# Optimization experiments

Hardware: AMD Instinct MI355X
Metric: run time of the kernel (lower is better)

The kernel has to match this reference:

```python
import jax, jax.numpy as jnp
import numpy as np

N_ACTIVE = 200000   # active voxels
GRID = 96           # spatial grid extent per axis
C = 128             # inplanes == outplanes
EPS = 1e-4          # scn BatchNormalization default eps


def _build_rulebook(n, g, seed=0):
    """Submanifold 3x3x3 rulebook: for each of 27 offsets, pairs (in_site, out_site)
    where coord[in] = coord[out] + offset and both sites are active. Padded to
    length n with dummy index n."""
    rng = np.random.default_rng(seed)
    lin = rng.choice(g ** 3, size=n, replace=False)
    coords = np.stack(np.unravel_index(lin, (g, g, g)), axis=1)  # [n,3]
    lut = -np.ones(g ** 3, dtype=np.int64)
    lut[lin] = np.arange(n)
    in_rows, out_rows = [], []
    for dx in (-1, 0, 1):
        for dy in (-1, 0, 1):
            for dz in (-1, 0, 1):
                nb = coords + np.array([dx, dy, dz])
                valid = np.all((nb >= 0) & (nb < g), axis=1)
                j = np.full(n, -1, dtype=np.int64)
                j[valid] = lut[np.ravel_multi_index(nb[valid].T, (g, g, g))]
                hit = j >= 0
                ii = j[hit]
                oi = np.nonzero(hit)[0].astype(np.int64)
                pad = n - ii.shape[0]
                in_rows.append(np.concatenate([ii, np.full(pad, n, dtype=np.int64)]))
                out_rows.append(np.concatenate([oi, np.full(pad, n, dtype=np.int64)]))
    return np.stack(in_rows), np.stack(out_rows)  # each [27, n]


def setup_inputs() -> dict:
    key = jax.random.key(0)
    k_feat, k_w1, k_w2 = jax.random.split(key, 3)
    in_idx_np, out_idx_np = _build_rulebook(N_ACTIVE, GRID)
    w_std = 1.0 / np.sqrt(27 * C)
    return {
        "features": jax.random.normal(k_feat, (N_ACTIVE, C), dtype=jnp.float32),
        "W1": jax.random.normal(k_w1, (27, C, C), dtype=jnp.float32) * w_std,
        "gamma1": jnp.ones((C,), jnp.float32),
        "beta1": jnp.zeros((C,), jnp.float32),
        "W2": jax.random.normal(k_w2, (27, C, C), dtype=jnp.float32) * w_std,
        "gamma2": jnp.ones((C,), jnp.float32),
        "beta2": jnp.zeros((C,), jnp.float32),
        "in_idx": jnp.asarray(in_idx_np),
        "out_idx": jnp.asarray(out_idx_np),
    }


def _subm_conv(feats, W, in_idx, out_idx):
    # feats: [N, Cin]; W: [27, Cin, Cout]; rulebook idx: [27, K] (dummy = N)
    n, c_in = feats.shape
    c_out = W.shape[-1]
    feats_pad = jnp.concatenate([feats, jnp.zeros((1, c_in), feats.dtype)], axis=0)

    def step(acc, t):
        ii, oi, w = t
        contrib = feats_pad[ii] @ w  # [K, Cout] gather -> GEMM
        return acc.at[oi].add(contrib), None  # scatter-add (dummy row n absorbs pad)

    acc0 = jnp.zeros((n + 1, c_out), feats.dtype)
    acc, _ = jax.lax.scan(step, acc0, (in_idx, out_idx, W))
    return acc[:n]


def _bn(x, gamma, beta):
    # batch-norm over active sites (training-mode batch stats)
    m = x.mean(axis=0)
    v = x.var(axis=0)
    return (x - m) * jax.lax.rsqrt(v + EPS) * gamma + beta


def reference(features, W1, gamma1, beta1, W2, gamma2, beta2, in_idx, out_idx):
    out = _subm_conv(features, W1, in_idx, out_idx)
    out = jax.nn.relu(_bn(out, gamma1, beta1))          # scn.BatchNormReLU
    out = _subm_conv(out, W2, in_idx, out_idx)
    out = _bn(out, gamma2, beta2)                       # scn.BatchNormalization
    return jax.nn.relu(out + features)                  # AddTable + ReLU
```

## Files before the change

### kernel.cpp

```cpp
#include <hip/hip_runtime.h>

#define NACT 200000
#define MPAD 200192
#define BM 256
#define NBLK 782
#define KOFF 27

#define NB_FILL 21114
#define NB_CAST 25001
#define NB_PREPW 1728
#define NB_PREP (NB_FILL + NB_CAST + NB_PREPW + 1)

typedef __bf16 bf16x8 __attribute__((ext_vector_type(8)));
typedef __bf16 bf16x4 __attribute__((ext_vector_type(4)));
typedef float f32x4 __attribute__((ext_vector_type(4)));

__device__ __forceinline__ void async_load16(const void* g, void* l) {
  __builtin_amdgcn_global_load_lds(
      (__attribute__((address_space(1))) void*)g,
      (__attribute__((address_space(3))) void*)l, 16, 0, 0);
}

__global__ void prep(int* __restrict__ G, const float* __restrict__ F,
                     __bf16* __restrict__ X, const float* __restrict__ W1,
                     const float* __restrict__ W2, __bf16* __restrict__ T1,
                     __bf16* __restrict__ T2, float* __restrict__ st) {
  const int b = blockIdx.x, t = threadIdx.x;
  if (b < NB_FILL) {
    int i = b * 256 + t;
    G[i] = NACT;
  } else if (b < NB_FILL + NB_CAST) {
    int i = (b - NB_FILL) * 256 + t;
    if (i >= (NACT + 1) * 32) return;
    float4 v = (i < NACT * 32) ? ((const float4*)F)[i] : make_float4(0.f, 0.f, 0.f, 0.f);
    bf16x4 o = {(__bf16)v.x, (__bf16)v.y, (__bf16)v.z, (__bf16)v.w};
    *(bf16x4*)(X + (i << 2)) = o;
  } else if (b < NB_FILL + NB_CAST + NB_PREPW) {
    int i = (b - NB_FILL - NB_CAST) * 256 + t;
    int k = i >> 14, rem = i & 16383, n = rem >> 7, c = rem & 127;
    int src = (k << 14) + (c << 7) + n;
    T1[i] = (__bf16)W1[src];
    T2[i] = (__bf16)W2[src];
  } else {
    if (t < 512) st[t] = 0.f;
  }
}

__global__ void scatter_g(const int* __restrict__ ii, const int* __restrict__ oi,
                          int* __restrict__ G) {
  int i = blockIdx.x * 256 + threadIdx.x;
  if (i >= KOFF * NACT) return;
  int k = i / NACT;
  int o = oi[i];
  if (o < NACT) G[(size_t)k * MPAD + o] = ii[i];
}

__global__ __launch_bounds__(512, 4) void gemm_gather(
    const __bf16* __restrict__ X,
    const __bf16* __restrict__ WT,
    const int* __restrict__ G,
    __bf16* __restrict__ Y,
    float* __restrict__ st)
{
  __shared__ __bf16 Alds[BM * 64];
  __shared__ __bf16 Blds[128 * 64];
  const int t = threadIdx.x;
  const int lane = t & 63;
  const int w = t >> 6;
  const int wm = (w & 3) << 6;
  const int wn = (w >> 2) << 6;
  const int m_base = blockIdx.x << 8;
  const int r0 = t >> 3;
  const int scb = t & 7;
  const int l15 = lane & 15;
  const int q4 = lane >> 4;

  f32x4 acc[4][4];
#pragma unroll
  for (int i = 0; i < 4; ++i)
#pragma unroll
    for (int j = 0; j < 4; ++j) acc[i][j] = (f32x4){0.f, 0.f, 0.f, 0.f};

  for (int kk = 0; kk < KOFF; ++kk) {
    int rowA[4];
#pragma unroll
    for (int j = 0; j < 4; ++j)
      rowA[j] = G[(size_t)kk * MPAD + m_base + r0 + j * 64];
    const __bf16* wb = WT + (kk << 14);
#pragma unroll
    for (int s = 0; s < 2; ++s) {
      const int c0 = s << 6;
      __syncthreads();
#pragma unroll
      for (int j = 0; j < 2; ++j) {
        const int r = r0 + j * 64;
        const int gcb = scb ^ (r & 7);
        async_load16(wb + (r << 7) + c0 + (gcb << 3), &Blds[(((r << 3) + scb) << 3)]);
      }
#pragma unroll
      for (int j = 0; j < 4; ++j) {
        const int r = r0 + j * 64;
        const int gcb = scb ^ (r & 7);
        async_load16(X + ((size_t)rowA[j] << 7) + c0 + (gcb << 3),
                     &Alds[(((r << 3) + scb) << 3)]);
      }
      __syncthreads();
#pragma unroll
      for (int ks = 0; ks < 2; ++ks) {
        bf16x8 af[4], bfr[4];
        const int cb0 = (ks << 2) + q4;
#pragma unroll
        for (int mi = 0; mi < 4; ++mi) {
          const int r = wm + mi * 16 + l15;
          af[mi] = *(const bf16x8*)&Alds[(((r << 3) + (cb0 ^ (r & 7))) << 3)];
        }
#pragma unroll
        for (int ni = 0; ni < 4; ++ni) {
          const int r = wn + ni * 16 + l15;
          bfr[ni] = *(const bf16x8*)&Blds[(((r << 3) + (cb0 ^ (r & 7))) << 3)];
        }
#pragma unroll
        for (int mi = 0; mi < 4; ++mi)
#pragma unroll
          for (int ni = 0; ni < 4; ++ni)
            acc[mi][ni] = __builtin_amdgcn_mfma_f32_16x16x32_bf16(
                af[mi], bfr[ni], acc[mi][ni], 0, 0, 0);
      }
    }
  }

#pragma unroll
  for (int mi = 0; mi < 4; ++mi) {
#pragma unroll
    for (int ni = 0; ni < 4; ++ni) {
      const int col = wn + ni * 16 + l15;
#pragma unroll
      for (int rg = 0; rg < 4; ++rg) {
        const int row = m_base + wm + mi * 16 + (q4 << 2) + rg;
        Y[((size_t)row << 7) + col] = (__bf16)acc[mi][ni][rg];
      }
    }
  }

  float s[4], s2[4];
#pragma unroll
  for (int ni = 0; ni < 4; ++ni) {
    float a = 0.f, b = 0.f;
#pragma unroll
    for (int mi = 0; mi < 4; ++mi)
#pragma unroll
      for (int rg = 0; rg < 4; ++rg) {
        float v = acc[mi][ni][rg];
        a += v; b += v * v;
      }
    s[ni] = a; s2[ni] = b;
  }
#pragma unroll
  for (int ni = 0; ni < 4; ++ni) {
    s[ni]  += __shfl_xor(s[ni], 16);  s[ni]  += __shfl_xor(s[ni], 32);
    s2[ni] += __shfl_xor(s2[ni], 16); s2[ni] += __shfl_xor(s2[ni], 32);
  }
  float* sc = (float*)Alds;
  __syncthreads();
  if (q4 == 0) {
#pragma unroll
    for (int ni = 0; ni < 4; ++ni) {
      sc[(w << 6) + ni * 16 + l15]       = s[ni];
      sc[512 + (w << 6) + ni * 16 + l15] = s2[ni];
    }
  }
  __syncthreads();
  if (t < 256) {
    const int kind = t >> 7, col = t & 127;
    const int wg = (col >> 6) << 2;
    const int c6 = col & 63;
    const float v = sc[kind * 512 + (wg + 0) * 64 + c6] +
                    sc[kind * 512 + (wg + 1) * 64 + c6] +
                    sc[kind * 512 + (wg + 2) * 64 + c6] +
                    sc[kind * 512 + (wg + 3) * 64 + c6];
    atomicAdd(&st[t], v);
  }
}

__global__ void bn_relu_cast(const __bf16* __restrict__ Y, const float* __restrict__ st,
                             const float* __restrict__ gamma, const float* __restrict__ beta,
                             __bf16* __restrict__ X2) {
  __shared__ float co[256];
  const int t = threadIdx.x;
  if (t < 128) {
    float m = st[t] * (1.f / NACT);
    float v = st[128 + t] * (1.f / NACT) - m * m;
    float sc = gamma[t] * rsqrtf(v + 1e-4f);
    co[t] = sc;
    co[128 + t] = beta[t] - m * sc;
  }
  __syncthreads();
  int i = blockIdx.x * 256 + t;
  if (i >= (NACT + 1) * 16) return;
  bf16x8 o;
  if (i < NACT * 16) {
    bf16x8 v = ((const bf16x8*)Y)[i];
    int cg = (i & 15) << 3;
#pragma unroll
    for (int e = 0; e < 8; ++e) {
      float x = fmaf((float)v[e], co[cg + e], co[128 + cg + e]);
      o[e] = (__bf16)fmaxf(x, 0.f);
    }
  } else {
#pragma unroll
    for (int e = 0; e < 8; ++e) o[e] = (__bf16)0.f;
  }
  ((bf16x8*)X2)[i] = o;
}

__global__ void bn_add_relu(const __bf16* __restrict__ Y, const float* __restrict__ st,
                            const float* __restrict__ gamma, const float* __restrict__ beta,
                            const float* __restrict__ F, float* __restrict__ O) {
  __shared__ float co[256];
  const int t = threadIdx.x;
  if (t < 128) {
    float m = st[t] * (1.f / NACT);
    float v = st[128 + t] * (1.f / NACT) - m * m;
    float sc = gamma[t] * rsqrtf(v + 1e-4f);
    co[t] = sc;
    co[128 + t] = beta[t] - m * sc;
  }
  __syncthreads();
  int i = blockIdx.x * 256 + t;
  if (i >= NACT * 16) return;
  bf16x8 v = ((const bf16x8*)Y)[i];
  float4 f0 = ((const float4*)F)[2 * i];
  float4 f1 = ((const float4*)F)[2 * i + 1];
  int cg = (i & 15) << 3;
  float4 o0, o1;
  o0.x = fmaxf(fmaf((float)v[0], co[cg + 0], co[128 + cg + 0]) + f0.x, 0.f);
  o0.y = fmaxf(fmaf((float)v[1], co[cg + 1], co[128 + cg + 1]) + f0.y, 0.f);
  o0.z = fmaxf(fmaf((float)v[2], co[cg + 2], co[128 + cg + 2]) + f0.z, 0.f);
  o0.w = fmaxf(fmaf((float)v[3], co[cg + 3], co[128 + cg + 3]) + f0.w, 0.f);
  o1.x = fmaxf(fmaf((float)v[4], co[cg + 4], co[128 + cg + 4]) + f1.x, 0.f);
  o1.y = fmaxf(fmaf((float)v[5], co[cg + 5], co[128 + cg + 5]) + f1.y, 0.f);
  o1.z = fmaxf(fmaf((float)v[6], co[cg + 6], co[128 + cg + 6]) + f1.z, 0.f);
  o1.w = fmaxf(fmaf((float)v[7], co[cg + 7], co[128 + cg + 7]) + f1.w, 0.f);
  ((float4*)O)[2 * i] = o0;
  ((float4*)O)[2 * i + 1] = o1;
}

extern "C" void kernel_launch(void* const* d_in, const int* in_sizes, int n_in,
                              void* d_out, int out_size, void* d_ws, size_t ws_size,
                              hipStream_t stream) {
  const float* features = (const float*)d_in[0];
  const float* W1       = (const float*)d_in[1];
  const float* gamma1   = (const float*)d_in[2];
  const float* beta1    = (const float*)d_in[3];
  const float* W2       = (const float*)d_in[4];
  const float* gamma2   = (const float*)d_in[5];
  const float* beta2    = (const float*)d_in[6];
  const int* in_idx     = (const int*)d_in[7];
  const int* out_idx    = (const int*)d_in[8];

  char* ws = (char*)d_ws;
  size_t off = 0;
  int*    G   = (int*)(ws + off);    off += (size_t)KOFF * MPAD * 4;
  __bf16* X   = (__bf16*)(ws + off); off += (size_t)(NACT + 1) * 128 * 2;
  __bf16* T1  = (__bf16*)(ws + off); off += (size_t)KOFF * 128 * 128 * 2;
  __bf16* T2  = (__bf16*)(ws + off); off += (size_t)KOFF * 128 * 128 * 2;
  __bf16* Y   = (__bf16*)(ws + off); off += (size_t)MPAD * 128 * 2;
  float*  st  = (float*)(ws + off);  off += 4096;

  prep<<<NB_PREP, 256, 0, stream>>>(G, features, X, W1, W2, T1, T2, st);
  scatter_g<<<(KOFF * NACT + 255) / 256, 256, 0, stream>>>(in_idx, out_idx, G);

  gemm_gather<<<NBLK, 512, 0, stream>>>(X, T1, G, Y, st);
  bn_relu_cast<<<((NACT + 1) * 16 + 255) / 256, 256, 0, stream>>>(Y, st, gamma1, beta1, X);

  gemm_gather<<<NBLK, 512, 0, stream>>>(X, T2, G, Y, st + 256);
  bn_add_relu<<<(NACT * 16 + 255) / 256, 256, 0, stream>>>(Y, st + 256, gamma2, beta2,
                                                           features, (float*)d_out);
}
```

Baseline: 618.3 us.

## Triple-buffer gather-GEMM LDS tiles with prefetch of indices and async loads

Restructures the gather-GEMM main loop into a flat sequence of 54 half-K tiles. A three-slot LDS ring lets the async global-to-LDS loads for tile s+2 and the rulebook index reads for tile s+3 be issued while tile s is computed. Raw s_barrier calls with scheduling barriers replace __syncthreads, and launch bounds drop to one block per CU to fit the larger LDS footprint. The aim is to hide gather latency behind MFMA work. The cost is much lower occupancy, and the code relies on the compiler's wait counts around the barriers for correctness and overlap.

Result: slower. 969.8 us (+56.8%).

```diff
diff --git a/kernel.cpp b/kernel.cpp
--- a/kernel.cpp
+++ b/kernel.cpp
@@ -5,6 +5,7 @@
 #define BM 256
 #define NBLK 782
 #define KOFF 27
+#define NTILE 54
 
 #define NB_FILL 21114
 #define NB_CAST 25001
@@ -55,15 +56,15 @@
   if (o < NACT) G[(size_t)k * MPAD + o] = ii[i];
 }
 
-__global__ __launch_bounds__(512, 4) void gemm_gather(
+__global__ __launch_bounds__(512, 1) void gemm_gather(
     const __bf16* __restrict__ X,
     const __bf16* __restrict__ WT,
     const int* __restrict__ G,
     __bf16* __restrict__ Y,
     float* __restrict__ st)
 {
-  __shared__ __bf16 Alds[BM * 64];
-  __shared__ __bf16 Blds[128 * 64];
+  __shared__ __bf16 Al[3][BM * 64];
+  __shared__ __bf16 Bl[3][128 * 64];
   const int t = threadIdx.x;
   const int lane = t & 63;
   const int w = t >> 6;
@@ -81,53 +82,76 @@
 #pragma unroll
     for (int j = 0; j < 4; ++j) acc[i][j] = (f32x4){0.f, 0.f, 0.f, 0.f};
 
-  for (int kk = 0; kk < KOFF; ++kk) {
-    int rowA[4];
-#pragma unroll
-    for (int j = 0; j < 4; ++j)
-      rowA[j] = G[(size_t)kk * MPAD + m_base + r0 + j * 64];
-    const __bf16* wb = WT + (kk << 14);
-#pragma unroll
-    for (int s = 0; s < 2; ++s) {
-      const int c0 = s << 6;
-      __syncthreads();
-#pragma unroll
-      for (int j = 0; j < 2; ++j) {
-        const int r = r0 + j * 64;
-        const int gcb = scb ^ (r & 7);
-        async_load16(wb + (r << 7) + c0 + (gcb << 3), &Blds[(((r << 3) + scb) << 3)]);
+#define GR(q, dst)                                                             \
+  do {                                                                         \
+    const int kq_ = (q) >> 1;                                                  \
+    _Pragma("unroll") for (int j = 0; j < 4; ++j)                              \
+        dst[j] = G[(size_t)kq_ * MPAD + m_base + r0 + j * 64];                 \
+  } while (0)
+
+#define ST(q, rows)                                                            \
+  do {                                                                         \
+    const int kq_ = (q) >> 1;                                                  \
+    const int c0_ = ((q) & 1) << 6;                                            \
+    const __bf16* wb_ = WT + (kq_ << 14);                                      \
+    __bf16* Ab_ = Al[(q) % 3];                                                 \
+    __bf16* Bb_ = Bl[(q) % 3];                                                 \
+    _Pragma("unroll") for (int j = 0; j < 2; ++j) {                            \
+      const int r_ = r0 + j * 64;                                              \
+      const int gcb_ = scb ^ (r_ & 7);                                         \
+      async_load16(wb_ + (r_ << 7) + c0_ + (gcb_ << 3),                        \
+                   &Bb_[(((r_ << 3) + scb) << 3)]);                            \
+    }                                                                          \
+    _Pragma("unroll") for (int j = 0; j < 4; ++j) {                            \
+      const int r_ = r0 + j * 64;                                              \
+      const int gcb_ = scb ^ (r_ & 7);                                         \
+      async_load16(X + ((size_t)rows[j] << 7) + c0_ + (gcb_ << 3),             \
+                   &Ab_[(((r_ << 3) + scb) << 3)]);                            \
+    }                                                                          \
+  } while (0)
+
+  int rA[4], rN[4];
+  GR(0, rA); ST(0, rA);
+  GR(1, rA); ST(1, rA);
+  GR(2, rA);
+
+  for (int s = 0; s < NTILE; ++s) {
+    if (s + 3 < NTILE) GR(s + 3, rN);
+    if (s + 2 < NTILE) ST(s + 2, rA);
+#pragma unroll
+    for (int j = 0; j < 4; ++j) rA[j] = rN[j];
+    __builtin_amdgcn_sched_barrier(0);
+    __builtin_amdgcn_s_barrier();
+    __builtin_amdgcn_sched_barrier(0);
+
+    const __bf16* Ab = Al[s % 3];
+    const __bf16* Bb = Bl[s % 3];
+#pragma unroll
+    for (int ks = 0; ks < 2; ++ks) {
+      bf16x8 af[4], bfr[4];
+      const int cb0 = (ks << 2) + q4;
+#pragma unroll
+      for (int mi = 0; mi < 4; ++mi) {
+        const int r = wm + mi * 16 + l15;
+        af[mi] = *(const bf16x8*)&Ab[(((r << 3) + (cb0 ^ (r & 7))) << 3)];
       }
 #pragma unroll
-      for (int j = 0; j < 4; ++j) {
-        const int r = r0 + j * 64;
-        const int gcb = scb ^ (r & 7);
-        async_load16(X + ((size_t)rowA[j] << 7) + c0 + (gcb << 3),
-                     &Alds[(((r << 3) + scb) << 3)]);
+      for (int ni = 0; ni < 4; ++ni) {
+        const int r = wn + ni * 16 + l15;
+        bfr[ni] = *(const bf16x8*)&Bb[(((r << 3) + (cb0 ^ (r & 7))) << 3)];
       }
-      __syncthreads();
-#pragma unroll
-      for (int ks = 0; ks < 2; ++ks) {
-        bf16x8 af[4], bfr[4];
-        const int cb0 = (ks << 2) + q4;
-#pragma unroll
-        for (int mi = 0; mi < 4; ++mi) {
-          const int r = wm + mi * 16 + l15;
-          af[mi] = *(const bf16x8*)&Alds[(((r << 3) + (cb0 ^ (r & 7))) << 3)];
-        }
-#pragma unroll
-        for (int ni = 0; ni < 4; ++ni) {
-          const int r = wn + ni * 16 + l15;
-          bfr[ni] = *(const bf16x8*)&Blds[(((r << 3) + (cb0 ^ (r & 7))) << 3)];
-        }
-#pragma unroll
-        for (int mi = 0; mi < 4; ++mi)
-#pragma unroll
-          for (int ni = 0; ni < 4; ++ni)
-            acc[mi][ni] = __builtin_amdgcn_mfma_f32_16x16x32_bf16(
-                af[mi], bfr[ni], acc[mi][ni], 0, 0, 0);
-      }
+#pragma unroll
+      for (int mi = 0; mi < 4; ++mi)
+#pragma unroll
+        for (int ni = 0; ni < 4; ++ni)
+          acc[mi][ni] = __builtin_amdgcn_mfma_f32_16x16x32_bf16(
+              af[mi], bfr[ni], acc[mi][ni], 0, 0, 0);
     }
-  }
+    __builtin_amdgcn_sched_barrier(0);
+    __builtin_amdgcn_s_barrier();
+  }
+#undef GR
+#undef ST
 
 #pragma unroll
   for (int mi = 0; mi < 4; ++mi) {
@@ -142,7 +166,7 @@
     }
   }
 
-  float s[4], s2[4];
+  float s1[4], s2[4];
 #pragma unroll
   for (int ni = 0; ni < 4; ++ni) {
     float a = 0.f, b = 0.f;
@@ -153,19 +177,19 @@
         float v = acc[mi][ni][rg];
         a += v; b += v * v;
       }
-    s[ni] = a; s2[ni] = b;
+    s1[ni] = a; s2[ni] = b;
   }
 #pragma unroll
   for (int ni = 0; ni < 4; ++ni) {
-    s[ni]  += __shfl_xor(s[ni], 16);  s[ni]  += __shfl_xor(s[ni], 32);
+    s1[ni] += __shfl_xor(s1[ni], 16); s1[ni] += __shfl_xor(s1[ni], 32);
     s2[ni] += __shfl_xor(s2[ni], 16); s2[ni] += __shfl_xor(s2[ni], 32);
   }
-  float* sc = (float*)Alds;
+  float* sc = (float*)Al;
   __syncthreads();
   if (q4 == 0) {
 #pragma unroll
     for (int ni = 0; ni < 4; ++ni) {
-      sc[(w << 6) + ni * 16 + l15]       = s[ni];
+      sc[(w << 6) + ni * 16 + l15]       = s1[ni];
       sc[512 + (w << 6) + ni * 16 + l15] = s2[ni];
     }
   }
```
